# Kernel optimization log

Hardware: AMD Instinct MI355X
Metric: run time of the kernel (lower is better)

Reference implementation:

```python
import jax, jax.numpy as jnp
import numpy as np

# ---- constants matching the original module's globals ----
H = 16          # self.h: number of bit levels; self.n = h per the source
TP = 8          # self.tp: parallel coordinate channels
N_K = 2         # random masks per flipped bit
T = 512         # T_train: tokens per block
N_TRNBR = 128   # neighbor count
K_VOCAB = 128   # sampled vocab count
N_VOCAB = 50257 # full vocab size V for sampled softmax correction
D = 256         # embedding dim
RATIO_COS = 1.0
RATIO_CRO = 0.1
C_CNC = 2 * H * N_K + 1  # candidate locations per token = 65


def setup_inputs() -> dict:
    key = jax.random.key(0)
    ks = jax.random.split(key, 8)
    n = H  # code: self.n = h
    sta_loc = jax.random.randint(ks[0], (T, TP), 1 - n, n, dtype=jnp.int32)
    nei_loc = jax.random.randint(ks[1], (T, N_TRNBR, TP), 1 - n, n, dtype=jnp.int32)
    voc_loc = jax.random.randint(ks[2], (T, K_VOCAB, TP), 1 - n, n, dtype=jnp.int32)
    sta_emb = jax.random.normal(ks[3], (T, D), dtype=jnp.float32)
    nei_emb = jax.random.normal(ks[4], (T, N_TRNBR, D), dtype=jnp.float32)
    voc_emb = jax.random.normal(ks[5], (T, K_VOCAB, D), dtype=jnp.float32)
    # raw random numbers for generate_random_masks: randint(0, self.n)
    rand_masks = jax.random.randint(ks[6], (T, H, N_K, TP), 0, n, dtype=jnp.int32)
    # converge mode: mask is all ones (generate_mask with converge=True)
    mask = jnp.ones((T, N_TRNBR), dtype=bool)
    return {"sta_loc": sta_loc, "nei_loc": nei_loc, "voc_loc": voc_loc,
            "sta_emb": sta_emb, "nei_emb": nei_emb, "voc_emb": voc_emb,
            "rand_masks": rand_masks, "mask": mask}


def _cos_similarity(c1, c2):
    # sign product: (+1 if >=0 else -1) for each operand
    sg = ((2 * (c1 >= 0).astype(jnp.int32) - 1) *
          (2 * (c2 >= 0).astype(jnp.int32) - 1)).astype(jnp.float32)
    x = ((jnp.abs(c1) ^ jnp.abs(c2)) + 1).astype(jnp.float32)
    # torch.frexp exponent of v>=1 equals floor(log2(v)) + 1
    expo = jnp.floor(jnp.log2(x)) + 1.0
    return sg * (1.0 - expo / H)


def _connection(sta_loc, rand_masks):
    bits = jnp.arange(H, dtype=jnp.int32)
    flip_masks = (1 << bits)                          # [H]
    flipped = sta_loc[:, None, :] ^ flip_masks[None, :, None]  # [T,H,TP]
    # note operator precedence in source: rn & (2**i - 1)
    rm = rand_masks & (flip_masks - 1)[None, :, None, None]    # [T,H,N_K,TP]
    res = (flipped[:, :, None, :] ^ rm).reshape(sta_loc.shape[0], H * N_K, TP)
    return jnp.concatenate([res, sta_loc[:, None, :], -res], axis=1)  # [T,C,TP]


def _normalize(x):
    return x / jnp.maximum(jnp.linalg.norm(x, axis=-1, keepdims=True), 1e-12)


def reference(sta_loc, nei_loc, voc_loc, sta_emb, nei_emb, voc_emb, rand_masks, mask):
    cnc_loc = _connection(sta_loc, rand_masks)          # [T, C, TP]
    lth = mask.sum(axis=1).astype(jnp.float32) + 1e-12  # [T]

    # euclidean-space cosine targets: [T, N_trnbr]
    eu_cos_val = jnp.einsum('td,tnd->tn', _normalize(sta_emb), _normalize(nei_emb))
    # use_eu_norm == True branch: ||sta|| * ||voc|| -> [T, K_vocab]
    eu_cro_nrm = (jnp.linalg.norm(sta_emb, axis=-1, keepdims=True) *
                  jnp.linalg.norm(voc_emb, axis=-1))

    pos_loc = jnp.concatenate([nei_loc, voc_loc], axis=1)           # [T, P, TP]
    cos_sta_pos = _cos_similarity(sta_loc[:, None, :], pos_loc)     # [T, P, TP]
    cos_sta_pos_sum = cos_sta_pos.sum(axis=-1)                      # [T, P]
    cos_cnc_pos = _cos_similarity(cnc_loc[:, None, :, :], pos_loc[:, :, None, :])  # [T,P,C,TP]
    ct_val = (cos_sta_pos_sum[:, :, None, None]
              - cos_sta_pos[:, :, None, :] + cos_cnc_pos) / TP      # [T,P,C,TP]

    # cosine-matching loss over neighbors
    eu = eu_cos_val[:, :, None, None]                               # [T,N,1,1]
    loss_cos = ((ct_val[:, :N_TRNBR] - eu) ** 2 * jnp.abs(eu)
                * mask[:, :, None, None].astype(jnp.float32))
    loss_cos = loss_cos.sum(axis=1) / lth[:, None, None]            # [T, C, TP]

    # sampled softmax CE (uniform proposal), positive class at vocab index 0
    z = ct_val[:, N_TRNBR:] * eu_cro_nrm[:, :, None, None]          # [T, K, C, TP]
    corr = jnp.where(jnp.arange(K_VOCAB) == 0, 0.0,
                     jnp.log(N_VOCAB / K_VOCAB)).astype(jnp.float32)
    zc = z + corr[None, :, None, None]
    loss_cro = jax.scipy.special.logsumexp(zc, axis=1) - zc[:, 0]   # [T, C, TP]

    loss_tot = RATIO_COS * loss_cos + RATIO_CRO * loss_cro

    # get_best_loc with cur_portion=1.0, cur_tp=tp -> pure argmin selection
    idx = jnp.argmin(loss_tot, axis=1)                              # [T, TP]
    gather = lambda a: jnp.take_along_axis(a, idx[:, None, :], axis=1)[:, 0]
    selected_locs = gather(cnc_loc)                                 # [T, TP]
    real_loss_cos = gather(loss_cos).mean(axis=-1)                  # [T]
    real_loss_cro = gather(loss_cro).mean(axis=-1)
    real_loss_tot = gather(loss_tot).mean(axis=-1)
    return selected_locs, real_loss_cos, real_loss_cro, real_loss_tot
```

## Files before the change

kernel.cpp:

```cpp
#include <hip/hip_runtime.h>
#include <math.h>

#define T_DIM 512
#define TP 8
#define NC 65
#define NJ 128
#define BLOCK 576
#define LOG2E 1.4426950408889634f
#define LN2   0.6931471805599453f
#define CORR_L2 8.617045f
#define WSTRIDE (NC * TP)

__device__ __forceinline__ float i2f(int x) { return __int_as_float(x); }
__device__ __forceinline__ int   f2i(float x) { return __float_as_int(x); }

__device__ __forceinline__ int cand_v(int c, int sta, const int* s_rand, int p) {
    if (c == 32) return sta;
    const int cc = (c < 32) ? c : (c - 33);
    const int h = cc >> 1;
    const int r = (sta ^ (1 << h)) ^ (s_rand[cc * TP + p] & ((1 << h) - 1));
    return (c < 32) ? r : -r;
}

#define CRO_Z(va, vs, X) ({                                             \
    const int _x = (va) ^ (X).x;                                        \
    const float _u0 = fmaf((float)__clz(_x + 1), 0.0625f, -1.0f);       \
    const float _u = i2f(f2i(_u0) ^ ((vs) ^ (X).y));                    \
    fmaf(_u, i2f((X).w), i2f((X).z));                                   \
})

__device__ __forceinline__ float cro_body1(int va, int vs, const int4* pc, float M) {
    const int4 x0 = pc[0];
    const float z0 = CRO_Z(va, vs, x0) - M;
    float s0 = __builtin_amdgcn_exp2f(z0);
    const int4 x1 = pc[8];
    float s1 = __builtin_amdgcn_exp2f(CRO_Z(va, vs, x1) - M);
    #pragma unroll 2
    for (int k = 2; k < NJ; k += 2) {
        const int4 x = pc[k * 8];
        const int4 y = pc[(k + 1) * 8];
        s0 += __builtin_amdgcn_exp2f(CRO_Z(va, vs, x) - M);
        s1 += __builtin_amdgcn_exp2f(CRO_Z(va, vs, y) - M);
    }
    const float S = fmaxf(s0 + s1, 1e-38f);
    return (__builtin_amdgcn_logf(S) - z0) * LN2;
}

__global__ __launch_bounds__(BLOCK, 5) void cg_side(
    const int* __restrict__ sta_loc,
    const int* __restrict__ nei_loc,
    const int* __restrict__ voc_loc,
    const float* __restrict__ sta_emb,
    const float* __restrict__ nei_emb,
    const float* __restrict__ voc_emb,
    const int* __restrict__ rand_masks,
    float* __restrict__ wcos,
    float* __restrict__ wcro)
{
    const int bid = blockIdx.x;
    const int side = bid & 1;
    const int t = bid >> 1;
    const int tid = threadIdx.x;

    __shared__ int4   s_pc4[NJ * TP];
    __shared__ float  s_cspT[TP * 132];
    __shared__ float  s_css[NJ];
    __shared__ float  s_dot[NJ];
    __shared__ float  s_nn[NJ];
    __shared__ float  s_Mpart[9 * 8];
    __shared__ float  s_ss;
    __shared__ int    s_sta[TP];
    __shared__ int    s_rand[256];
    __shared__ int    s_qs[NJ * TP];
    __shared__ float  s_eu[NJ];
    __shared__ float2 s_U[TP][17];
    __shared__ float  s_G[TP];

    if (tid < 256) s_rand[tid] = rand_masks[t * 256 + tid];

    if (tid < 512) {
        const int g = tid >> 2, sub = tid & 3;
        const float4* sp = (const float4*)(sta_emb + (size_t)t * 256);
        const float* emb = side ? voc_emb : nei_emb;
        const float4* ep = (const float4*)(emb + ((size_t)t * NJ + g) * 256);
        float dd = 0.f, nn = 0.f, ss = 0.f;
        #pragma unroll 4
        for (int i = 0; i < 16; ++i) {
            const int i4 = sub + 4 * i;
            const float4 b = ep[i4];
            nn += b.x * b.x + b.y * b.y + b.z * b.z + b.w * b.w;
            if (side == 0 || g == 0) {
                const float4 a = sp[i4];
                if (side == 0) dd += a.x * b.x + a.y * b.y + a.z * b.z + a.w * b.w;
                if (g == 0)    ss += a.x * a.x + a.y * a.y + a.z * a.z + a.w * a.w;
            }
        }
        nn += __shfl_xor(nn, 1); nn += __shfl_xor(nn, 2);
        if (side == 0) { dd += __shfl_xor(dd, 1); dd += __shfl_xor(dd, 2); }
        if (g == 0) { ss += __shfl_xor(ss, 1); ss += __shfl_xor(ss, 2); }
        if (sub == 0) {
            s_nn[g] = nn;
            if (side == 0) s_dot[g] = dd;
            if (g == 0) s_ss = ss;
        }
    } else {
        const int l = tid - 512;
        if (l < TP) s_sta[l] = sta_loc[t * TP + l];
        const int4 sta4 = ((const int4*)(sta_loc + t * TP))[l & 1];
        const int sarr[4] = {sta4.x, sta4.y, sta4.z, sta4.w};
        const int* loc = side ? voc_loc : nei_loc;
        const int4* lp = (const int4*)(loc + (size_t)t * 1024);
        #pragma unroll
        for (int q = 0; q < 4; ++q) {
            const int4 pl4 = lp[q * 64 + l];
            const int j = q * 32 + (l >> 1);
            const int parr[4] = {pl4.x, pl4.y, pl4.z, pl4.w};
            float cs4 = 0.f;
            #pragma unroll
            for (int e = 0; e < 4; ++e) {
                const int pl = parr[e];
                const int sta = sarr[e];
                const int idx = q * 256 + 4 * l + e;
                const int qa = pl < 0 ? -pl : pl;
                const int qsgn = pl & 0x80000000;
                const int sa = sta < 0 ? -sta : sta;
                const int x = sa ^ qa;
                const float u0 = fmaf((float)__clz(x + 1), 0.0625f, -1.0f);
                const float csp = i2f(f2i(u0) ^ ((sta ^ pl) & 0x80000000));
                if (side) ((int2*)&s_pc4[idx])[0] = make_int2(qa, qsgn);
                else      s_qs[idx] = qa | qsgn;
                s_cspT[(4 * (l & 1) + e) * 132 + j] = csp;
                cs4 += csp;
            }
            const float cs8 = cs4 + __shfl_xor(cs4, 1);
            if (!(l & 1)) s_css[j] = cs8;
        }
    }
    __syncthreads();

    if (side == 0) {
        if (tid < NJ) {
            const float ns = fmaxf(sqrtf(s_ss), 1e-12f);
            s_eu[tid] = s_dot[tid] / (fmaxf(sqrtf(s_nn[tid]), 1e-12f) * ns);
        }
        __syncthreads();

        if (tid < 512) {
            const int p = tid >> 6;
            const int chunk = (tid >> 4) & 3;
            const int q = tid & 15;
            float u1 = 0.f, u0 = 0.f, g = 0.f;
            const int jb = chunk * 32;
            #pragma unroll 4
            for (int i = 0; i < 32; ++i) {
                const int j = jb + i;
                const int qs = s_qs[j * TP + p];
                const float csp = s_cspT[p * 132 + j];
                const float b = s_css[j] - csp;
                const float eu = s_eu[j];
                const float B = fmaf(b, 0.125f, -eu);
                const float w = fabsf(eu);
                const float wB = w * B;
                g = fmaf(wB, B, g);
                const bool hit = (qs & 15) == q;
                u1 += hit ? i2f(f2i(wB) ^ (qs & 0x80000000)) : 0.f;
                u0 += hit ? w : 0.f;
            }
            u1 += __shfl_xor(u1, 16); u1 += __shfl_xor(u1, 32);
            u0 += __shfl_xor(u0, 16); u0 += __shfl_xor(u0, 32);
            g  += __shfl_xor(g, 16);  g  += __shfl_xor(g, 32);
            if (chunk == 0) {
                s_U[p][q] = make_float2(u1, u0);
                if (q == 0) s_G[p] = g;
            }
        }
        __syncthreads();

        if (tid < NC * TP) {
            const int c = tid >> 3, p = tid & 7;
            const int v = cand_v(c, s_sta[p], s_rand, p);
            const int va = v < 0 ? -v : v;
            const int svb = v & 0x80000000;
            float S1 = 0.f, S0 = 0.f;
            #pragma unroll
            for (int q = 0; q < 16; ++q) {
                const float2 uv = s_U[p][q];
                const int x = va ^ q;
                const float m = fmaf((float)__clz(x + 1), 0.0625f, -1.0f);
                S1 = fmaf(m, uv.x, S1);
                S0 = fmaf(m * m, uv.y, S0);
            }
            const float lc = (s_G[p] + i2f(f2i(0.25f * S1) ^ svb)
                              + 0.015625f * S0) * 0.0078125f;
            wcos[t * WSTRIDE + c * TP + p] = lc;
        }
    } else {
        {
            const float ns = sqrtf(s_ss);
            float mloc = -INFINITY;
            #pragma unroll
            for (int k = 0; k < 2; ++k) {
                const int item = tid + k * BLOCK;
                if (item < 1024) {
                    const int j = item >> 3;
                    const int p = item & 7;
                    const float csp = s_cspT[p * 132 + j];
                    const float b = s_css[j] - csp;
                    const float A = ns * sqrtf(s_nn[j]) * (0.125f * LOG2E);
                    const float z2 = fmaf(b, A, j ? CORR_L2 : 0.0f);
                    mloc = fmaxf(mloc, z2 + A);
                    ((int2*)&s_pc4[item])[1] = make_int2(f2i(z2), f2i(A));
                }
            }
            mloc = fmaxf(mloc, __shfl_xor(mloc, 8));
            mloc = fmaxf(mloc, __shfl_xor(mloc, 16));
            mloc = fmaxf(mloc, __shfl_xor(mloc, 32));
            const int lane = tid & 63;
            if (lane < 8) s_Mpart[(tid >> 6) * 8 + lane] = mloc;
        }
        __syncthreads();

        if (tid < NC * TP) {
            const int c = tid >> 3, p = tid & 7;
            const int v = cand_v(c, s_sta[p], s_rand, p);
            float M = s_Mpart[p];
            #pragma unroll
            for (int wv = 1; wv < 9; ++wv) M = fmaxf(M, s_Mpart[wv * 8 + p]);
            wcro[t * WSTRIDE + c * TP + p] =
                cro_body1(v < 0 ? -v : v, v & 0x80000000, s_pc4 + p, M);
        }
    }
}

__global__ void cg_combine(
    const int* __restrict__ sta_loc,
    const int* __restrict__ rand_masks,
    const float* __restrict__ wcos,
    const float* __restrict__ wcro,
    float* __restrict__ out)
{
    const int t = blockIdx.x;
    const int tid = threadIdx.x;
    const int p = tid & 7, cg = tid >> 3;

    float best = INFINITY, blc = 0.f, blr = 0.f;
    int bc = NC;
    for (int c = cg; c < NC; c += 8) {
        const float lc = wcos[t * WSTRIDE + c * TP + p];
        const float lr = wcro[t * WSTRIDE + c * TP + p];
        const float lt = fmaf(0.1f, lr, lc);
        if (lt < best) { best = lt; bc = c; blc = lc; blr = lr; }
    }
    #pragma unroll
    for (int d = 8; d < 64; d <<= 1) {
        const float o_best = __shfl_xor(best, d);
        const float o_blc  = __shfl_xor(blc, d);
        const float o_blr  = __shfl_xor(blr, d);
        const int   o_bc   = __shfl_xor(bc, d);
        if (o_best < best || (o_best == best && o_bc < bc)) {
            best = o_best; bc = o_bc; blc = o_blc; blr = o_blr;
        }
    }

    float vc = 0.f, vr = 0.f, vt = 0.f;
    if (tid < TP) {
        const int sta = sta_loc[t * TP + tid];
        out[t * TP + tid] = (float)cand_v(bc, sta, rand_masks + t * 256, tid);
        vc = blc; vr = blr; vt = best;
    }
    vc += __shfl_xor(vc, 1); vc += __shfl_xor(vc, 2); vc += __shfl_xor(vc, 4);
    vr += __shfl_xor(vr, 1); vr += __shfl_xor(vr, 2); vr += __shfl_xor(vr, 4);
    vt += __shfl_xor(vt, 1); vt += __shfl_xor(vt, 2); vt += __shfl_xor(vt, 4);
    if (tid == 0) {
        out[T_DIM * TP + t] = vc * 0.125f;
        out[T_DIM * TP + T_DIM + t] = vr * 0.125f;
        out[T_DIM * TP + 2 * T_DIM + t] = vt * 0.125f;
    }
}

extern "C" void kernel_launch(void* const* d_in, const int* in_sizes, int n_in,
                              void* d_out, int out_size, void* d_ws, size_t ws_size,
                              hipStream_t stream) {
    const int* sta_loc = (const int*)d_in[0];
    const int* nei_loc = (const int*)d_in[1];
    const int* voc_loc = (const int*)d_in[2];
    const float* sta_emb = (const float*)d_in[3];
    const float* nei_emb = (const float*)d_in[4];
    const float* voc_emb = (const float*)d_in[5];
    const int* rand_masks = (const int*)d_in[6];
    float* out = (float*)d_out;

    float* wcos = (float*)d_ws;
    float* wcro = wcos + (size_t)WSTRIDE * T_DIM;

    cg_side<<<2 * T_DIM, BLOCK, 0, stream>>>(
        sta_loc, nei_loc, voc_loc, sta_emb, nei_emb, voc_emb, rand_masks,
        wcos, wcro);
    cg_combine<<<T_DIM, 64, 0, stream>>>(sta_loc, rand_masks, wcos, wcro, out);
}
```

Before: 193.4 us.

## Merge neighbor and vocab sides into one block per token with register prefetch

Replaces the two-blocks-per-token split (one block for the neighbor cosine side, one for the vocab cross-entropy side) with a single 512-thread block per token that runs both sides in sequence. The vocab embedding rows are prefetched into registers while the cosine-side work runs, so that global load latency overlaps with computation, and the start-token embedding is staged once in shared memory. The cost is more registers per thread (sixteen float4 prefetch values), a lower occupancy hint, and half as many blocks to keep the GPU busy. The candidate loops now need a second pass, since 520 items exceed 512 threads.

```diff
diff --git a/kernel.cpp b/kernel.cpp
--- a/kernel.cpp
+++ b/kernel.cpp
@@ -5,7 +5,7 @@
 #define TP 8
 #define NC 65
 #define NJ 128
-#define BLOCK 576
+#define BLOCK 512
 #define LOG2E 1.4426950408889634f
 #define LN2   0.6931471805599453f
 #define CORR_L2 8.617045f
@@ -46,7 +46,7 @@
     return (__builtin_amdgcn_logf(S) - z0) * LN2;
 }
 
-__global__ __launch_bounds__(BLOCK, 5) void cg_side(
+__global__ __launch_bounds__(BLOCK, 4) void cg_t(
     const int* __restrict__ sta_loc,
     const int* __restrict__ nei_loc,
     const int* __restrict__ voc_loc,
@@ -57,178 +57,186 @@
     float* __restrict__ wcos,
     float* __restrict__ wcro)
 {
-    const int bid = blockIdx.x;
-    const int side = bid & 1;
-    const int t = bid >> 1;
+    const int t = blockIdx.x;
     const int tid = threadIdx.x;
 
     __shared__ int4   s_pc4[NJ * TP];
-    __shared__ float  s_cspT[TP * 132];
-    __shared__ float  s_css[NJ];
+    __shared__ float  s_cspT[2][TP * 132];
+    __shared__ float  s_css[2][NJ];
     __shared__ float  s_dot[NJ];
     __shared__ float  s_nn[NJ];
-    __shared__ float  s_Mpart[9 * 8];
+    __shared__ float  s_eu[NJ];
+    __shared__ float2 s_U[TP][17];
+    __shared__ float  s_G[TP];
+    __shared__ float  s_Mpart[8 * 8];
     __shared__ float  s_ss;
     __shared__ int    s_sta[TP];
     __shared__ int    s_rand[256];
     __shared__ int    s_qs[NJ * TP];
-    __shared__ float  s_eu[NJ];
-    __shared__ float2 s_U[TP][17];
-    __shared__ float  s_G[TP];
+    __shared__ float4 s_a[64];
 
     if (tid < 256) s_rand[tid] = rand_masks[t * 256 + tid];
-
-    if (tid < 512) {
-        const int g = tid >> 2, sub = tid & 3;
-        const float4* sp = (const float4*)(sta_emb + (size_t)t * 256);
-        const float* emb = side ? voc_emb : nei_emb;
-        const float4* ep = (const float4*)(emb + ((size_t)t * NJ + g) * 256);
+    if (tid < TP)  s_sta[tid] = sta_loc[t * TP + tid];
+    if (tid < 64)  s_a[tid] = ((const float4*)(sta_emb + (size_t)t * 256))[tid];
+
+    const int half = tid >> 8;
+    const int li = tid & 255;
+    const int4 l4 = ((const int4*)((half ? voc_loc : nei_loc)
+                                   + (size_t)t * 1024))[li];
+    const int4 sta4 = ((const int4*)(sta_loc + t * TP))[li & 1];
+
+    const int g = tid >> 2, sub = tid & 3;
+    const float4* np = (const float4*)(nei_emb + ((size_t)t * NJ + g) * 256);
+    const float4* vp = (const float4*)(voc_emb + ((size_t)t * NJ + g) * 256);
+    float4 pf[16];
+    #pragma unroll
+    for (int i = 0; i < 16; ++i) pf[i] = np[sub + 4 * i];
+
+    {
+        const int j = li >> 1, ph = li & 1;
+        const int sarr[4] = {sta4.x, sta4.y, sta4.z, sta4.w};
+        const int parr[4] = {l4.x, l4.y, l4.z, l4.w};
+        float cs4 = 0.f;
+        #pragma unroll
+        for (int e = 0; e < 4; ++e) {
+            const int pl = parr[e];
+            const int sta = sarr[e];
+            const int idx = 8 * j + 4 * ph + e;
+            const int qa = pl < 0 ? -pl : pl;
+            const int qsgn = pl & 0x80000000;
+            const int sa = sta < 0 ? -sta : sta;
+            const int x = sa ^ qa;
+            const float u0 = fmaf((float)__clz(x + 1), 0.0625f, -1.0f);
+            const float csp = i2f(f2i(u0) ^ ((sta ^ pl) & 0x80000000));
+            if (half) ((int2*)&s_pc4[idx])[0] = make_int2(qa, qsgn);
+            else      s_qs[idx] = qa | qsgn;
+            s_cspT[half][(4 * ph + e) * 132 + j] = csp;
+            cs4 += csp;
+        }
+        const float cs8 = cs4 + __shfl_xor(cs4, 1);
+        if (!(li & 1)) s_css[half][j] = cs8;
+    }
+    __syncthreads();
+
+    {
         float dd = 0.f, nn = 0.f, ss = 0.f;
-        #pragma unroll 4
+        #pragma unroll
         for (int i = 0; i < 16; ++i) {
-            const int i4 = sub + 4 * i;
-            const float4 b = ep[i4];
+            const float4 a = s_a[sub + 4 * i];
+            const float4 b = pf[i];
             nn += b.x * b.x + b.y * b.y + b.z * b.z + b.w * b.w;
-            if (side == 0 || g == 0) {
-                const float4 a = sp[i4];
-                if (side == 0) dd += a.x * b.x + a.y * b.y + a.z * b.z + a.w * b.w;
-                if (g == 0)    ss += a.x * a.x + a.y * a.y + a.z * a.z + a.w * a.w;
-            }
-        }
+            dd += a.x * b.x + a.y * b.y + a.z * b.z + a.w * b.w;
+            if (g == 0) ss += a.x * a.x + a.y * a.y + a.z * a.z + a.w * a.w;
+        }
+        #pragma unroll
+        for (int i = 0; i < 16; ++i) pf[i] = vp[sub + 4 * i];
         nn += __shfl_xor(nn, 1); nn += __shfl_xor(nn, 2);
-        if (side == 0) { dd += __shfl_xor(dd, 1); dd += __shfl_xor(dd, 2); }
+        dd += __shfl_xor(dd, 1); dd += __shfl_xor(dd, 2);
         if (g == 0) { ss += __shfl_xor(ss, 1); ss += __shfl_xor(ss, 2); }
         if (sub == 0) {
-            s_nn[g] = nn;
-            if (side == 0) s_dot[g] = dd;
+            s_nn[g] = nn; s_dot[g] = dd;
             if (g == 0) s_ss = ss;
         }
-    } else {
-        const int l = tid - 512;
-        if (l < TP) s_sta[l] = sta_loc[t * TP + l];
-        const int4 sta4 = ((const int4*)(sta_loc + t * TP))[l & 1];
-        const int sarr[4] = {sta4.x, sta4.y, sta4.z, sta4.w};
-        const int* loc = side ? voc_loc : nei_loc;
-        const int4* lp = (const int4*)(loc + (size_t)t * 1024);
-        #pragma unroll
-        for (int q = 0; q < 4; ++q) {
-            const int4 pl4 = lp[q * 64 + l];
-            const int j = q * 32 + (l >> 1);
-            const int parr[4] = {pl4.x, pl4.y, pl4.z, pl4.w};
-            float cs4 = 0.f;
-            #pragma unroll
-            for (int e = 0; e < 4; ++e) {
-                const int pl = parr[e];
-                const int sta = sarr[e];
-                const int idx = q * 256 + 4 * l + e;
-                const int qa = pl < 0 ? -pl : pl;
-                const int qsgn = pl & 0x80000000;
-                const int sa = sta < 0 ? -sta : sta;
-                const int x = sa ^ qa;
-                const float u0 = fmaf((float)__clz(x + 1), 0.0625f, -1.0f);
-                const float csp = i2f(f2i(u0) ^ ((sta ^ pl) & 0x80000000));
-                if (side) ((int2*)&s_pc4[idx])[0] = make_int2(qa, qsgn);
-                else      s_qs[idx] = qa | qsgn;
-                s_cspT[(4 * (l & 1) + e) * 132 + j] = csp;
-                cs4 += csp;
-            }
-            const float cs8 = cs4 + __shfl_xor(cs4, 1);
-            if (!(l & 1)) s_css[j] = cs8;
-        }
-    }
-    __syncthreads();
-
-    if (side == 0) {
-        if (tid < NJ) {
-            const float ns = fmaxf(sqrtf(s_ss), 1e-12f);
-            s_eu[tid] = s_dot[tid] / (fmaxf(sqrtf(s_nn[tid]), 1e-12f) * ns);
-        }
-        __syncthreads();
-
-        if (tid < 512) {
-            const int p = tid >> 6;
-            const int chunk = (tid >> 4) & 3;
-            const int q = tid & 15;
-            float u1 = 0.f, u0 = 0.f, g = 0.f;
-            const int jb = chunk * 32;
-            #pragma unroll 4
-            for (int i = 0; i < 32; ++i) {
-                const int j = jb + i;
-                const int qs = s_qs[j * TP + p];
-                const float csp = s_cspT[p * 132 + j];
-                const float b = s_css[j] - csp;
-                const float eu = s_eu[j];
-                const float B = fmaf(b, 0.125f, -eu);
-                const float w = fabsf(eu);
-                const float wB = w * B;
-                g = fmaf(wB, B, g);
-                const bool hit = (qs & 15) == q;
-                u1 += hit ? i2f(f2i(wB) ^ (qs & 0x80000000)) : 0.f;
-                u0 += hit ? w : 0.f;
-            }
-            u1 += __shfl_xor(u1, 16); u1 += __shfl_xor(u1, 32);
-            u0 += __shfl_xor(u0, 16); u0 += __shfl_xor(u0, 32);
-            g  += __shfl_xor(g, 16);  g  += __shfl_xor(g, 32);
-            if (chunk == 0) {
-                s_U[p][q] = make_float2(u1, u0);
-                if (q == 0) s_G[p] = g;
-            }
-        }
-        __syncthreads();
-
-        if (tid < NC * TP) {
-            const int c = tid >> 3, p = tid & 7;
-            const int v = cand_v(c, s_sta[p], s_rand, p);
-            const int va = v < 0 ? -v : v;
-            const int svb = v & 0x80000000;
-            float S1 = 0.f, S0 = 0.f;
-            #pragma unroll
-            for (int q = 0; q < 16; ++q) {
-                const float2 uv = s_U[p][q];
-                const int x = va ^ q;
-                const float m = fmaf((float)__clz(x + 1), 0.0625f, -1.0f);
-                S1 = fmaf(m, uv.x, S1);
-                S0 = fmaf(m * m, uv.y, S0);
-            }
-            const float lc = (s_G[p] + i2f(f2i(0.25f * S1) ^ svb)
-                              + 0.015625f * S0) * 0.0078125f;
-            wcos[t * WSTRIDE + c * TP + p] = lc;
-        }
-    } else {
-        {
-            const float ns = sqrtf(s_ss);
-            float mloc = -INFINITY;
-            #pragma unroll
-            for (int k = 0; k < 2; ++k) {
-                const int item = tid + k * BLOCK;
-                if (item < 1024) {
-                    const int j = item >> 3;
-                    const int p = item & 7;
-                    const float csp = s_cspT[p * 132 + j];
-                    const float b = s_css[j] - csp;
-                    const float A = ns * sqrtf(s_nn[j]) * (0.125f * LOG2E);
-                    const float z2 = fmaf(b, A, j ? CORR_L2 : 0.0f);
-                    mloc = fmaxf(mloc, z2 + A);
-                    ((int2*)&s_pc4[item])[1] = make_int2(f2i(z2), f2i(A));
-                }
-            }
-            mloc = fmaxf(mloc, __shfl_xor(mloc, 8));
-            mloc = fmaxf(mloc, __shfl_xor(mloc, 16));
-            mloc = fmaxf(mloc, __shfl_xor(mloc, 32));
-            const int lane = tid & 63;
-            if (lane < 8) s_Mpart[(tid >> 6) * 8 + lane] = mloc;
-        }
-        __syncthreads();
-
-        if (tid < NC * TP) {
-            const int c = tid >> 3, p = tid & 7;
-            const int v = cand_v(c, s_sta[p], s_rand, p);
-            float M = s_Mpart[p];
-            #pragma unroll
-            for (int wv = 1; wv < 9; ++wv) M = fmaxf(M, s_Mpart[wv * 8 + p]);
-            wcro[t * WSTRIDE + c * TP + p] =
-                cro_body1(v < 0 ? -v : v, v & 0x80000000, s_pc4 + p, M);
-        }
+    }
+    __syncthreads();
+
+    if (tid < NJ) {
+        const float ns = fmaxf(sqrtf(s_ss), 1e-12f);
+        s_eu[tid] = s_dot[tid] / (fmaxf(sqrtf(s_nn[tid]), 1e-12f) * ns);
+    }
+    __syncthreads();
+
+    {
+        const int p = tid >> 6;
+        const int chunk = (tid >> 4) & 3;
+        const int q = tid & 15;
+        float u1 = 0.f, u0 = 0.f, gg = 0.f;
+        const int jb = chunk * 32;
+        #pragma unroll 4
+        for (int i = 0; i < 32; ++i) {
+            const int j = jb + i;
+            const int qs = s_qs[j * TP + p];
+            const float csp = s_cspT[0][p * 132 + j];
+            const float b = s_css[0][j] - csp;
+            const float eu = s_eu[j];
+            const float B = fmaf(b, 0.125f, -eu);
+            const float w = fabsf(eu);
+            const float wB = w * B;
+            gg = fmaf(wB, B, gg);
+            const bool hit = (qs & 15) == q;
+            u1 += hit ? i2f(f2i(wB) ^ (qs & 0x80000000)) : 0.f;
+            u0 += hit ? w : 0.f;
+        }
+        u1 += __shfl_xor(u1, 16); u1 += __shfl_xor(u1, 32);
+        u0 += __shfl_xor(u0, 16); u0 += __shfl_xor(u0, 32);
+        gg += __shfl_xor(gg, 16); gg += __shfl_xor(gg, 32);
+        if (chunk == 0) {
+            s_U[p][q] = make_float2(u1, u0);
+            if (q == 0) s_G[p] = gg;
+        }
+    }
+    __syncthreads();
+
+    for (int item = tid; item < NC * TP; item += BLOCK) {
+        const int c = item >> 3, p = item & 7;
+        const int v = cand_v(c, s_sta[p], s_rand, p);
+        const int va = v < 0 ? -v : v;
+        const int svb = v & 0x80000000;
+        float S1 = 0.f, S0 = 0.f;
+        #pragma unroll
+        for (int q = 0; q < 16; ++q) {
+            const float2 uv = s_U[p][q];
+            const int x = va ^ q;
+            const float m = fmaf((float)__clz(x + 1), 0.0625f, -1.0f);
+            S1 = fmaf(m, uv.x, S1);
+            S0 = fmaf(m * m, uv.y, S0);
+        }
+        wcos[t * WSTRIDE + c * TP + p] =
+            (s_G[p] + i2f(f2i(0.25f * S1) ^ svb) + 0.015625f * S0) * 0.0078125f;
+    }
+
+    {
+        float nn = 0.f;
+        #pragma unroll
+        for (int i = 0; i < 16; ++i) {
+            const float4 b = pf[i];
+            nn += b.x * b.x + b.y * b.y + b.z * b.z + b.w * b.w;
+        }
+        nn += __shfl_xor(nn, 1); nn += __shfl_xor(nn, 2);
+        if (sub == 0) s_nn[g] = nn;
+    }
+    __syncthreads();
+
+    {
+        const float ns = sqrtf(s_ss);
+        float mloc = -INFINITY;
+        #pragma unroll
+        for (int k = 0; k < 2; ++k) {
+            const int item = tid + k * BLOCK;
+            const int j = item >> 3;
+            const int p = item & 7;
+            const float csp = s_cspT[1][p * 132 + j];
+            const float b = s_css[1][j] - csp;
+            const float A = ns * sqrtf(s_nn[j]) * (0.125f * LOG2E);
+            const float z2 = fmaf(b, A, j ? CORR_L2 : 0.0f);
+            mloc = fmaxf(mloc, z2 + A);
+            ((int2*)&s_pc4[item])[1] = make_int2(f2i(z2), f2i(A));
+        }
+        mloc = fmaxf(mloc, __shfl_xor(mloc, 8));
+        mloc = fmaxf(mloc, __shfl_xor(mloc, 16));
+        mloc = fmaxf(mloc, __shfl_xor(mloc, 32));
+        if ((tid & 63) < 8) s_Mpart[(tid >> 6) * 8 + (tid & 7)] = mloc;
+    }
+    __syncthreads();
+
+    for (int item = tid; item < NC * TP; item += BLOCK) {
+        const int c = item >> 3, p = item & 7;
+        const int v = cand_v(c, s_sta[p], s_rand, p);
+        float M = s_Mpart[p];
+        #pragma unroll
+        for (int wv = 1; wv < 8; ++wv) M = fmaxf(M, s_Mpart[wv * 8 + p]);
+        wcro[t * WSTRIDE + c * TP + p] =
+            cro_body1(v < 0 ? -v : v, v & 0x80000000, s_pc4 + p, M);
     }
 }
 
@@ -293,7 +301,7 @@
     float* wcos = (float*)d_ws;
     float* wcro = wcos + (size_t)WSTRIDE * T_DIM;
 
-    cg_side<<<2 * T_DIM, BLOCK, 0, stream>>>(
+    cg_t<<<T_DIM, BLOCK, 0, stream>>>(
         sta_loc, nei_loc, voc_loc, sta_emb, nei_emb, voc_emb, rand_masks,
         wcos, wcro);
     cg_combine<<<T_DIM, 64, 0, stream>>>(sta_loc, rand_masks, wcos, wcro, out);
```

New measurement: 195.2 us. Within noise of the previous version (+0.9%).

## Split neighbor/vocab dimension into four chunks with partial log-sum-exp combine

Applied to the files above, without the earlier changes.

The main kernel now splits the 128 neighbor/vocab entries into four chunks of 32, launching 4x more blocks of 256 threads instead of one 576-thread block per token and side. Each chunk writes partial cosine sums, partial exp sums and chunk maxima to the workspace. The combine kernel merges them using the standard rescaled log-sum-exp. This aims to raise parallelism and occupancy and to shorten the serial 128-iteration softmax loop. The cost is extra workspace traffic and redundant per-block setup work such as the rand mask loads and the sta norm.

```diff
diff --git a/kernel.cpp b/kernel.cpp
--- a/kernel.cpp
+++ b/kernel.cpp
@@ -5,7 +5,9 @@
 #define TP 8
 #define NC 65
 #define NJ 128
-#define BLOCK 576
+#define NCH 4
+#define CJ 32
+#define BLOCK 256
 #define LOG2E 1.4426950408889634f
 #define LN2   0.6931471805599453f
 #define CORR_L2 8.617045f
@@ -29,24 +31,7 @@
     fmaf(_u, i2f((X).w), i2f((X).z));                                   \
 })
 
-__device__ __forceinline__ float cro_body1(int va, int vs, const int4* pc, float M) {
-    const int4 x0 = pc[0];
-    const float z0 = CRO_Z(va, vs, x0) - M;
-    float s0 = __builtin_amdgcn_exp2f(z0);
-    const int4 x1 = pc[8];
-    float s1 = __builtin_amdgcn_exp2f(CRO_Z(va, vs, x1) - M);
-    #pragma unroll 2
-    for (int k = 2; k < NJ; k += 2) {
-        const int4 x = pc[k * 8];
-        const int4 y = pc[(k + 1) * 8];
-        s0 += __builtin_amdgcn_exp2f(CRO_Z(va, vs, x) - M);
-        s1 += __builtin_amdgcn_exp2f(CRO_Z(va, vs, y) - M);
-    }
-    const float S = fmaxf(s0 + s1, 1e-38f);
-    return (__builtin_amdgcn_logf(S) - z0) * LN2;
-}
-
-__global__ __launch_bounds__(BLOCK, 5) void cg_side(
+__global__ __launch_bounds__(BLOCK, 8) void cg_chunk(
     const int* __restrict__ sta_loc,
     const int* __restrict__ nei_loc,
     const int* __restrict__ voc_loc,
@@ -55,130 +40,126 @@
     const float* __restrict__ voc_emb,
     const int* __restrict__ rand_masks,
     float* __restrict__ wcos,
-    float* __restrict__ wcro)
+    float* __restrict__ wS,
+    float* __restrict__ wM,
+    float* __restrict__ wz0)
 {
     const int bid = blockIdx.x;
-    const int side = bid & 1;
-    const int t = bid >> 1;
+    const int t = bid & (T_DIM - 1);
+    const int side = (bid >> 9) & 1;
+    const int chunk = bid >> 10;
+    const int j0 = chunk * CJ;
     const int tid = threadIdx.x;
-
-    __shared__ int4   s_pc4[NJ * TP];
-    __shared__ float  s_cspT[TP * 132];
-    __shared__ float  s_css[NJ];
-    __shared__ float  s_dot[NJ];
-    __shared__ float  s_nn[NJ];
-    __shared__ float  s_Mpart[9 * 8];
-    __shared__ float  s_ss;
-    __shared__ int    s_sta[TP];
-    __shared__ int    s_rand[256];
-    __shared__ int    s_qs[NJ * TP];
-    __shared__ float  s_eu[NJ];
+    const int w = tid >> 6, lane = tid & 63;
+    const int jl = tid >> 3, p = tid & 7;
+
+    __shared__ float  s_dot[CJ];
+    __shared__ float  s_nn[CJ];
+    __shared__ float  s_css[CJ];
+    __shared__ float  s_cspT[TP][CJ + 1];
+    __shared__ float  s_eu[CJ];
+    __shared__ int    s_qs[CJ * TP];
+    __shared__ int4   s_pc4[CJ * TP];
     __shared__ float2 s_U[TP][17];
     __shared__ float  s_G[TP];
-
-    if (tid < 256) s_rand[tid] = rand_masks[t * 256 + tid];
-
-    if (tid < 512) {
-        const int g = tid >> 2, sub = tid & 3;
-        const float4* sp = (const float4*)(sta_emb + (size_t)t * 256);
-        const float* emb = side ? voc_emb : nei_emb;
-        const float4* ep = (const float4*)(emb + ((size_t)t * NJ + g) * 256);
-        float dd = 0.f, nn = 0.f, ss = 0.f;
-        #pragma unroll 4
-        for (int i = 0; i < 16; ++i) {
-            const int i4 = sub + 4 * i;
-            const float4 b = ep[i4];
-            nn += b.x * b.x + b.y * b.y + b.z * b.z + b.w * b.w;
-            if (side == 0 || g == 0) {
-                const float4 a = sp[i4];
-                if (side == 0) dd += a.x * b.x + a.y * b.y + a.z * b.z + a.w * b.w;
-                if (g == 0)    ss += a.x * a.x + a.y * a.y + a.z * a.z + a.w * a.w;
-            }
-        }
-        nn += __shfl_xor(nn, 1); nn += __shfl_xor(nn, 2);
-        if (side == 0) { dd += __shfl_xor(dd, 1); dd += __shfl_xor(dd, 2); }
-        if (g == 0) { ss += __shfl_xor(ss, 1); ss += __shfl_xor(ss, 2); }
-        if (sub == 0) {
-            s_nn[g] = nn;
-            if (side == 0) s_dot[g] = dd;
-            if (g == 0) s_ss = ss;
-        }
-    } else {
-        const int l = tid - 512;
-        if (l < TP) s_sta[l] = sta_loc[t * TP + l];
-        const int4 sta4 = ((const int4*)(sta_loc + t * TP))[l & 1];
-        const int sarr[4] = {sta4.x, sta4.y, sta4.z, sta4.w};
-        const int* loc = side ? voc_loc : nei_loc;
-        const int4* lp = (const int4*)(loc + (size_t)t * 1024);
-        #pragma unroll
-        for (int q = 0; q < 4; ++q) {
-            const int4 pl4 = lp[q * 64 + l];
-            const int j = q * 32 + (l >> 1);
-            const int parr[4] = {pl4.x, pl4.y, pl4.z, pl4.w};
-            float cs4 = 0.f;
+    __shared__ float  s_Mpart[4][TP];
+    __shared__ int    s_rand[256];
+
+    s_rand[tid] = rand_masks[t * 256 + tid];
+
+    const float4 a = ((const float4*)(sta_emb + (size_t)t * 256))[lane];
+    float ss = a.x * a.x + a.y * a.y + a.z * a.z + a.w * a.w;
+    ss += __shfl_xor(ss, 1);  ss += __shfl_xor(ss, 2);  ss += __shfl_xor(ss, 4);
+    ss += __shfl_xor(ss, 8);  ss += __shfl_xor(ss, 16); ss += __shfl_xor(ss, 32);
+
+    const float* emb = side ? voc_emb : nei_emb;
+    const float4* ep = (const float4*)(emb + ((size_t)t * NJ + j0 + w * 8) * 256);
+
+    float4 bb[4];
+    #pragma unroll
+    for (int r = 0; r < 4; ++r) bb[r] = ep[r * 64 + lane];
+
+    const int sta = sta_loc[t * TP + p];
+    const int pl = (side ? voc_loc : nei_loc)[t * (NJ * TP) + (j0 + jl) * TP + p];
+    {
+        const int qa = pl < 0 ? -pl : pl;
+        const int qsgn = pl & 0x80000000;
+        const int sa = sta < 0 ? -sta : sta;
+        const int x = sa ^ qa;
+        const float u0 = fmaf((float)__clz(x + 1), 0.0625f, -1.0f);
+        const float csp = i2f(f2i(u0) ^ ((sta ^ pl) & 0x80000000));
+        if (side) ((int2*)&s_pc4[jl * TP + p])[0] = make_int2(qa, qsgn);
+        else      s_qs[jl * TP + p] = qa | qsgn;
+        s_cspT[p][jl] = csp;
+        float cs = csp;
+        cs += __shfl_xor(cs, 1); cs += __shfl_xor(cs, 2); cs += __shfl_xor(cs, 4);
+        if (p == 0) s_css[jl] = cs;
+    }
+
+    #pragma unroll
+    for (int r = 0; r < 4; ++r) {
+        const float4 b = bb[r];
+        float nn = b.x * b.x + b.y * b.y + b.z * b.z + b.w * b.w;
+        float dd = a.x * b.x + a.y * b.y + a.z * b.z + a.w * b.w;
+        nn += __shfl_xor(nn, 1);  nn += __shfl_xor(nn, 2);  nn += __shfl_xor(nn, 4);
+        nn += __shfl_xor(nn, 8);  nn += __shfl_xor(nn, 16); nn += __shfl_xor(nn, 32);
+        dd += __shfl_xor(dd, 1);  dd += __shfl_xor(dd, 2);  dd += __shfl_xor(dd, 4);
+        dd += __shfl_xor(dd, 8);  dd += __shfl_xor(dd, 16); dd += __shfl_xor(dd, 32);
+        if (lane == 0) { s_nn[w * 8 + r] = nn; s_dot[w * 8 + r] = dd; }
+    }
+    #pragma unroll
+    for (int r = 0; r < 4; ++r) bb[r] = ep[(4 + r) * 64 + lane];
+    #pragma unroll
+    for (int r = 0; r < 4; ++r) {
+        const float4 b = bb[r];
+        float nn = b.x * b.x + b.y * b.y + b.z * b.z + b.w * b.w;
+        float dd = a.x * b.x + a.y * b.y + a.z * b.z + a.w * b.w;
+        nn += __shfl_xor(nn, 1);  nn += __shfl_xor(nn, 2);  nn += __shfl_xor(nn, 4);
+        nn += __shfl_xor(nn, 8);  nn += __shfl_xor(nn, 16); nn += __shfl_xor(nn, 32);
+        dd += __shfl_xor(dd, 1);  dd += __shfl_xor(dd, 2);  dd += __shfl_xor(dd, 4);
+        dd += __shfl_xor(dd, 8);  dd += __shfl_xor(dd, 16); dd += __shfl_xor(dd, 32);
+        if (lane == 0) { s_nn[w * 8 + 4 + r] = nn; s_dot[w * 8 + 4 + r] = dd; }
+    }
+    __syncthreads();
+
+    if (side == 0) {
+        if (tid < CJ) {
+            const float ns = fmaxf(sqrtf(ss), 1e-12f);
+            s_eu[tid] = s_dot[tid] / (fmaxf(sqrtf(s_nn[tid]), 1e-12f) * ns);
+        }
+        __syncthreads();
+
+        {
+            const int pp = tid >> 5, half = (tid >> 4) & 1, q = tid & 15;
+            float u1 = 0.f, u0 = 0.f, gg = 0.f;
             #pragma unroll
-            for (int e = 0; e < 4; ++e) {
-                const int pl = parr[e];
-                const int sta = sarr[e];
-                const int idx = q * 256 + 4 * l + e;
-                const int qa = pl < 0 ? -pl : pl;
-                const int qsgn = pl & 0x80000000;
-                const int sa = sta < 0 ? -sta : sta;
-                const int x = sa ^ qa;
-                const float u0 = fmaf((float)__clz(x + 1), 0.0625f, -1.0f);
-                const float csp = i2f(f2i(u0) ^ ((sta ^ pl) & 0x80000000));
-                if (side) ((int2*)&s_pc4[idx])[0] = make_int2(qa, qsgn);
-                else      s_qs[idx] = qa | qsgn;
-                s_cspT[(4 * (l & 1) + e) * 132 + j] = csp;
-                cs4 += csp;
-            }
-            const float cs8 = cs4 + __shfl_xor(cs4, 1);
-            if (!(l & 1)) s_css[j] = cs8;
-        }
-    }
-    __syncthreads();
-
-    if (side == 0) {
-        if (tid < NJ) {
-            const float ns = fmaxf(sqrtf(s_ss), 1e-12f);
-            s_eu[tid] = s_dot[tid] / (fmaxf(sqrtf(s_nn[tid]), 1e-12f) * ns);
-        }
-        __syncthreads();
-
-        if (tid < 512) {
-            const int p = tid >> 6;
-            const int chunk = (tid >> 4) & 3;
-            const int q = tid & 15;
-            float u1 = 0.f, u0 = 0.f, g = 0.f;
-            const int jb = chunk * 32;
-            #pragma unroll 4
-            for (int i = 0; i < 32; ++i) {
-                const int j = jb + i;
-                const int qs = s_qs[j * TP + p];
-                const float csp = s_cspT[p * 132 + j];
+            for (int i = 0; i < 16; ++i) {
+                const int j = half * 16 + i;
+                const int qs = s_qs[j * TP + pp];
+                const float csp = s_cspT[pp][j];
                 const float b = s_css[j] - csp;
                 const float eu = s_eu[j];
                 const float B = fmaf(b, 0.125f, -eu);
-                const float w = fabsf(eu);
-                const float wB = w * B;
-                g = fmaf(wB, B, g);
+                const float ww = fabsf(eu);
+                const float wB = ww * B;
+                gg = fmaf(wB, B, gg);
                 const bool hit = (qs & 15) == q;
                 u1 += hit ? i2f(f2i(wB) ^ (qs & 0x80000000)) : 0.f;
-                u0 += hit ? w : 0.f;
-            }
-            u1 += __shfl_xor(u1, 16); u1 += __shfl_xor(u1, 32);
-            u0 += __shfl_xor(u0, 16); u0 += __shfl_xor(u0, 32);
-            g  += __shfl_xor(g, 16);  g  += __shfl_xor(g, 32);
-            if (chunk == 0) {
-                s_U[p][q] = make_float2(u1, u0);
-                if (q == 0) s_G[p] = g;
+                u0 += hit ? ww : 0.f;
+            }
+            u1 += __shfl_xor(u1, 16);
+            u0 += __shfl_xor(u0, 16);
+            gg += __shfl_xor(gg, 16);
+            if (half == 0) {
+                s_U[pp][q] = make_float2(u1, u0);
+                if (q == 0) s_G[pp] = gg;
             }
         }
         __syncthreads();
 
-        if (tid < NC * TP) {
-            const int c = tid >> 3, p = tid & 7;
-            const int v = cand_v(c, s_sta[p], s_rand, p);
+        for (int item = tid; item < WSTRIDE; item += BLOCK) {
+            const int c = item >> 3;
+            const int v = cand_v(c, sta, s_rand, p);
             const int va = v < 0 ? -v : v;
             const int svb = v & 0x80000000;
             float S1 = 0.f, S0 = 0.f;
@@ -190,44 +171,48 @@
                 S1 = fmaf(m, uv.x, S1);
                 S0 = fmaf(m * m, uv.y, S0);
             }
-            const float lc = (s_G[p] + i2f(f2i(0.25f * S1) ^ svb)
-                              + 0.015625f * S0) * 0.0078125f;
-            wcos[t * WSTRIDE + c * TP + p] = lc;
+            wcos[((size_t)chunk * T_DIM + t) * WSTRIDE + item] =
+                (s_G[p] + i2f(f2i(0.25f * S1) ^ svb) + 0.015625f * S0) * 0.0078125f;
         }
     } else {
         {
-            const float ns = sqrtf(s_ss);
-            float mloc = -INFINITY;
-            #pragma unroll
-            for (int k = 0; k < 2; ++k) {
-                const int item = tid + k * BLOCK;
-                if (item < 1024) {
-                    const int j = item >> 3;
-                    const int p = item & 7;
-                    const float csp = s_cspT[p * 132 + j];
-                    const float b = s_css[j] - csp;
-                    const float A = ns * sqrtf(s_nn[j]) * (0.125f * LOG2E);
-                    const float z2 = fmaf(b, A, j ? CORR_L2 : 0.0f);
-                    mloc = fmaxf(mloc, z2 + A);
-                    ((int2*)&s_pc4[item])[1] = make_int2(f2i(z2), f2i(A));
-                }
-            }
+            const float ns = sqrtf(ss);
+            const float csp = s_cspT[p][jl];
+            const float b = s_css[jl] - csp;
+            const float A = ns * sqrtf(s_nn[jl]) * (0.125f * LOG2E);
+            const float z2 = fmaf(b, A, (j0 + jl) ? CORR_L2 : 0.0f);
+            ((int2*)&s_pc4[jl * TP + p])[1] = make_int2(f2i(z2), f2i(A));
+            float mloc = z2 + A;
             mloc = fmaxf(mloc, __shfl_xor(mloc, 8));
             mloc = fmaxf(mloc, __shfl_xor(mloc, 16));
             mloc = fmaxf(mloc, __shfl_xor(mloc, 32));
-            const int lane = tid & 63;
-            if (lane < 8) s_Mpart[(tid >> 6) * 8 + lane] = mloc;
+            if (lane < 8) s_Mpart[w][lane] = mloc;
         }
         __syncthreads();
-
-        if (tid < NC * TP) {
-            const int c = tid >> 3, p = tid & 7;
-            const int v = cand_v(c, s_sta[p], s_rand, p);
-            float M = s_Mpart[p];
-            #pragma unroll
-            for (int wv = 1; wv < 9; ++wv) M = fmaxf(M, s_Mpart[wv * 8 + p]);
-            wcro[t * WSTRIDE + c * TP + p] =
-                cro_body1(v < 0 ? -v : v, v & 0x80000000, s_pc4 + p, M);
+        const float M = fmaxf(fmaxf(s_Mpart[0][p], s_Mpart[1][p]),
+                              fmaxf(s_Mpart[2][p], s_Mpart[3][p]));
+        if (tid < 8) wM[((size_t)chunk * T_DIM + t) * TP + tid] =
+            fmaxf(fmaxf(s_Mpart[0][tid], s_Mpart[1][tid]),
+                  fmaxf(s_Mpart[2][tid], s_Mpart[3][tid]));
+
+        for (int item = tid; item < WSTRIDE; item += BLOCK) {
+            const int c = item >> 3;
+            const int v = cand_v(c, sta, s_rand, p);
+            const int va = v < 0 ? -v : v;
+            const int vs = v & 0x80000000;
+            float s0 = 0.f, s1 = 0.f;
+            #pragma unroll 2
+            for (int k = 0; k < CJ; k += 2) {
+                const int4 X = s_pc4[k * TP + p];
+                const int4 Y = s_pc4[(k + 1) * TP + p];
+                s0 += __builtin_amdgcn_exp2f(CRO_Z(va, vs, X) - M);
+                s1 += __builtin_amdgcn_exp2f(CRO_Z(va, vs, Y) - M);
+            }
+            wS[((size_t)chunk * T_DIM + t) * WSTRIDE + item] = s0 + s1;
+            if (chunk == 0) {
+                const int4 X0 = s_pc4[p];
+                wz0[(size_t)t * WSTRIDE + item] = CRO_Z(va, vs, X0);
+            }
         }
     }
 }
@@ -236,18 +221,36 @@
     const int* __restrict__ sta_loc,
     const int* __restrict__ rand_masks,
     const float* __restrict__ wcos,
-    const float* __restrict__ wcro,
+    const float* __restrict__ wS,
+    const float* __restrict__ wM,
+    const float* __restrict__ wz0,
     float* __restrict__ out)
 {
     const int t = blockIdx.x;
     const int tid = threadIdx.x;
     const int p = tid & 7, cg = tid >> 3;
 
+    const float M0 = wM[((size_t)0 * T_DIM + t) * TP + p];
+    const float M1 = wM[((size_t)1 * T_DIM + t) * TP + p];
+    const float M2 = wM[((size_t)2 * T_DIM + t) * TP + p];
+    const float M3 = wM[((size_t)3 * T_DIM + t) * TP + p];
+    const float Ms = fmaxf(fmaxf(M0, M1), fmaxf(M2, M3));
+    const float e0 = __builtin_amdgcn_exp2f(M0 - Ms);
+    const float e1 = __builtin_amdgcn_exp2f(M1 - Ms);
+    const float e2 = __builtin_amdgcn_exp2f(M2 - Ms);
+    const float e3 = __builtin_amdgcn_exp2f(M3 - Ms);
+
     float best = INFINITY, blc = 0.f, blr = 0.f;
     int bc = NC;
     for (int c = cg; c < NC; c += 8) {
-        const float lc = wcos[t * WSTRIDE + c * TP + p];
-        const float lr = wcro[t * WSTRIDE + c * TP + p];
+        const size_t idx = (size_t)t * WSTRIDE + c * TP + p;
+        const size_t cs = (size_t)T_DIM * WSTRIDE;
+        const float lc = wcos[idx] + wcos[cs + idx]
+                       + wcos[2 * cs + idx] + wcos[3 * cs + idx];
+        const float S = wS[idx] * e0 + wS[cs + idx] * e1
+                      + wS[2 * cs + idx] * e2 + wS[3 * cs + idx] * e3;
+        const float lr = (__builtin_amdgcn_logf(fmaxf(S, 1e-38f))
+                          + Ms - wz0[idx]) * LN2;
         const float lt = fmaf(0.1f, lr, lc);
         if (lt < best) { best = lt; bc = c; blc = lc; blr = lr; }
     }
@@ -291,10 +294,13 @@
     float* out = (float*)d_out;
 
     float* wcos = (float*)d_ws;
-    float* wcro = wcos + (size_t)WSTRIDE * T_DIM;
-
-    cg_side<<<2 * T_DIM, BLOCK, 0, stream>>>(
+    float* wS   = wcos + (size_t)NCH * T_DIM * WSTRIDE;
+    float* wM   = wS   + (size_t)NCH * T_DIM * WSTRIDE;
+    float* wz0  = wM   + (size_t)NCH * T_DIM * TP;
+
+    cg_chunk<<<NCH * 2 * T_DIM, BLOCK, 0, stream>>>(
         sta_loc, nei_loc, voc_loc, sta_emb, nei_emb, voc_emb, rand_masks,
-        wcos, wcro);
-    cg_combine<<<T_DIM, 64, 0, stream>>>(sta_loc, rand_masks, wcos, wcro, out);
+        wcos, wS, wM, wz0);
+    cg_combine<<<T_DIM, 64, 0, stream>>>(
+        sta_loc, rand_masks, wcos, wS, wM, wz0, out);
 }
```

Result: faster. 178.7 us (-7.6%).
